# Optimization experiments

Measured on AMD Instinct MI355X. Metric: run time of the kernel, lower is better.

## Reference

```python
import jax, jax.numpy as jnp
import numpy as np

D_MODEL = 1024
H = 16
D_K = D_MODEL // H


def setup_inputs() -> dict:
    key = jax.random.key(0)
    ks = jax.random.split(key, 10)
    B, S = 2, 2048
    s = 1.0 / np.sqrt(D_MODEL)
    x = jax.random.normal(ks[0], (B, S, D_MODEL), dtype=jnp.float32)
    mask = jax.random.randint(ks[1], (B, 1, S, S), 0, 2, dtype=jnp.int32)
    w_q = jax.random.normal(ks[2], (D_MODEL, D_MODEL), dtype=jnp.float32) * s
    b_q = jnp.zeros((D_MODEL,), dtype=jnp.float32)
    w_k = jax.random.normal(ks[3], (D_MODEL, D_MODEL), dtype=jnp.float32) * s
    b_k = jnp.zeros((D_MODEL,), dtype=jnp.float32)
    w_v = jax.random.normal(ks[4], (D_MODEL, D_MODEL), dtype=jnp.float32) * s
    b_v = jnp.zeros((D_MODEL,), dtype=jnp.float32)
    w_o = jax.random.normal(ks[5], (D_MODEL, D_MODEL), dtype=jnp.float32) * s
    b_o = jnp.zeros((D_MODEL,), dtype=jnp.float32)
    return {"x": x, "mask": mask, "w_q": w_q, "b_q": b_q, "w_k": w_k,
            "b_k": b_k, "w_v": w_v, "b_v": b_v, "w_o": w_o, "b_o": b_o}


def reference(x, mask, w_q, b_q, w_k, b_k, w_v, b_v, w_o, b_o):
    B, S, _ = x.shape
    # projections; weights stored as (in, out) equivalents of torch Linear
    q = (x @ w_q + b_q).reshape(B, S, H, D_K).transpose(0, 2, 1, 3)  # bhsd
    k = (x @ w_k + b_k).reshape(B, S, H, D_K).transpose(0, 2, 1, 3)
    v = (x @ w_v + b_v).reshape(B, S, H, D_K).transpose(0, 2, 1, 3)
    scores = jnp.einsum('bhqd,bhkd->bhqk', q, k) / jnp.sqrt(jnp.float32(D_K))
    scores = jnp.where(mask == 0, jnp.float32(-1e9), scores)
    attn = jax.nn.softmax(scores, axis=-1)  # dropout omitted (eval mode)
    out = jnp.einsum('bhqk,bhkd->bhqd', attn, v)
    out = out.transpose(0, 2, 1, 3).reshape(B, S, D_MODEL)
    return out @ w_o + b_o
```

## Files before the change

### kernel.cpp

```cpp
#include <hip/hip_runtime.h>
#include <hip/hip_bf16.h>
#include <stdint.h>

#define D_MODEL 1024
#define NH 16
#define DK 64
#define SEQ 2048
#define BATCH 2
#define NTOK (BATCH * SEQ)

typedef __bf16 bf16;
typedef float f32x4 __attribute__((ext_vector_type(4)));
typedef __bf16 bf16x8 __attribute__((ext_vector_type(8)));
typedef __bf16 bf16x4 __attribute__((ext_vector_type(4)));

#define QSCALE 0.18033687932432668f

__device__ __forceinline__ void gload_lds16(const void* g, void* l) {
  __builtin_amdgcn_global_load_lds(
      (const __attribute__((address_space(1))) void*)g,
      (__attribute__((address_space(3))) void*)l, 16, 0, 0);
}

__global__ void prep_kernel(const float* __restrict__ x, bf16* __restrict__ xb,
                            const float* __restrict__ wq, const float* __restrict__ wk,
                            const float* __restrict__ wv, const float* __restrict__ wo,
                            bf16* __restrict__ wt,
                            const int* __restrict__ mask, unsigned long long* __restrict__ bits) {
  __shared__ float tile[32][33];
  const int bx = blockIdx.x;
  const int tid = threadIdx.x;
  if (bx < 4096) {
    int i = bx * 256 + tid;
    float4 v = reinterpret_cast<const float4*>(x)[i];
    bf16x4 o;
    o[0] = (bf16)v.x; o[1] = (bf16)v.y; o[2] = (bf16)v.z; o[3] = (bf16)v.w;
    reinterpret_cast<bf16x4*>(xb)[i] = o;
  } else if (bx < 8192) {
    int blk = bx - 4096;
    const int jt = blk & 127;
    const int kt = blk >> 7;
    const int tx = tid & 31, ty = tid >> 5;
    const int j0 = jt * 32;
    const int sel = j0 >> 10;
    const float* w = (sel == 0) ? wq : (sel == 1) ? wk : (sel == 2) ? wv : wo;
    const int jj0 = j0 & 1023;
#pragma unroll
    for (int i = 0; i < 4; ++i)
      tile[ty + i * 8][tx] = w[(size_t)(kt * 32 + ty + i * 8) * 1024 + jj0 + tx];
    __syncthreads();
#pragma unroll
    for (int i = 0; i < 4; ++i)
      wt[(size_t)(j0 + ty + i * 8) * 1024 + kt * 32 + tx] = (bf16)tile[tx][ty + i * 8];
  } else {
    int gt = (bx - 8192) * 256 + tid;
    int wid = gt >> 6;
    int l = gt & 63;
    int m = mask[(size_t)wid * 64 + l];
    unsigned long long b = __ballot(m != 0);
    if (l == 0) bits[wid] = b;
  }
}

__global__ __launch_bounds__(256) void gemm_qkv(
    const bf16* __restrict__ A, const bf16* __restrict__ Bt,
    const float* __restrict__ b0, const float* __restrict__ b1, const float* __restrict__ b2,
    bf16* __restrict__ out_q, bf16* __restrict__ out_k, bf16* __restrict__ out_vt) {
  __shared__ __align__(16) bf16 As[128 * 64];
  __shared__ __align__(16) bf16 Bs[128 * 64];
  const int tid = threadIdx.x;
  const int w = tid >> 6, l = tid & 63;
  const int wr = w >> 1, wc = w & 1;
  int lin = blockIdx.x + 24 * blockIdx.y;
  int xcd = lin & 7, idx = lin >> 3;
  const int n0 = (xcd * 3 + idx % 3) * 128;
  const int m0 = (idx / 3) * 128;
  f32x4 acc[4][4] = {};
  const int srow = w * 8 + (l >> 3);
  const int ssw = ((l & 7) ^ (l >> 3)) * 8;
  char* AsB = (char*)As;
  char* BsB = (char*)Bs;

  for (int k0 = 0; k0 < 1024; k0 += 64) {
#pragma unroll
    for (int i = 0; i < 4; ++i) {
      gload_lds16(A + (size_t)(m0 + i * 32 + srow) * 1024 + k0 + ssw, AsB + i * 4096 + w * 1024);
      gload_lds16(Bt + (size_t)(n0 + i * 32 + srow) * 1024 + k0 + ssw, BsB + i * 4096 + w * 1024);
    }
    __syncthreads();
#pragma unroll
    for (int kk = 0; kk < 2; ++kk) {
      const int cc = (((kk * 4 + (l >> 4)) ^ (l & 7)) << 3);
      bf16x8 af[4], bfr[4];
#pragma unroll
      for (int m = 0; m < 4; ++m)
        af[m] = *reinterpret_cast<const bf16x8*>(As + (wr * 64 + m * 16 + (l & 15)) * 64 + cc);
#pragma unroll
      for (int n = 0; n < 4; ++n)
        bfr[n] = *reinterpret_cast<const bf16x8*>(Bs + (wc * 64 + n * 16 + (l & 15)) * 64 + cc);
#pragma unroll
      for (int m = 0; m < 4; ++m)
#pragma unroll
        for (int n = 0; n < 4; ++n)
          acc[m][n] = __builtin_amdgcn_mfma_f32_16x16x32_bf16(af[m], bfr[n], acc[m][n], 0, 0, 0);
    }
    __syncthreads();
  }

#pragma unroll
  for (int m = 0; m < 4; ++m) {
    int ib = m0 + wr * 64 + m * 16 + 4 * (l >> 4);
#pragma unroll
    for (int n = 0; n < 4; ++n) {
      int j = n0 + wc * 64 + n * 16 + (l & 15);
      int sel = j >> 10, jj = j & 1023;
      const float* bp = (sel == 0) ? b0 : (sel == 1) ? b1 : b2;
      float bias = bp[jj];
      if (sel == 0) {
#pragma unroll
        for (int r = 0; r < 4; ++r)
          out_q[(size_t)(ib + r) * 1024 + jj] = (bf16)((acc[m][n][r] + bias) * QSCALE);
      } else if (sel == 1) {
#pragma unroll
        for (int r = 0; r < 4; ++r)
          out_k[(size_t)(ib + r) * 1024 + jj] = (bf16)(acc[m][n][r] + bias);
      } else {
        int hh = jj >> 6, dd = jj & 63;
        int bb = ib >> 11, ss = ib & 2047;
        bf16x4 v;
#pragma unroll
        for (int r = 0; r < 4; ++r) v[r] = (bf16)(acc[m][n][r] + bias);
        *reinterpret_cast<bf16x4*>(out_vt + ((size_t)(bb * NH + hh) * DK + dd) * SEQ + ss) = v;
      }
    }
  }
}

__global__ __launch_bounds__(256) void gemm_out(
    const bf16* __restrict__ A, const bf16* __restrict__ Bt,
    const float* __restrict__ bias, float* __restrict__ out) {
  __shared__ __align__(16) bf16 As[128 * 64];
  __shared__ __align__(16) bf16 Bs[64 * 64];
  const int tid = threadIdx.x;
  const int w = tid >> 6, l = tid & 63;
  const int wr = w >> 1, wc = w & 1;
  int lin = blockIdx.x + 16 * blockIdx.y;
  int xcd = lin & 7, idx = lin >> 3;
  const int n0 = (xcd * 2 + idx % 2) * 64;
  const int m0 = (idx / 2) * 128;
  f32x4 acc[4][2] = {};
  const int srow = w * 8 + (l >> 3);
  const int ssw = ((l & 7) ^ (l >> 3)) * 8;
  char* AsB = (char*)As;
  char* BsB = (char*)Bs;

  for (int k0 = 0; k0 < 1024; k0 += 64) {
#pragma unroll
    for (int i = 0; i < 4; ++i)
      gload_lds16(A + (size_t)(m0 + i * 32 + srow) * 1024 + k0 + ssw, AsB + i * 4096 + w * 1024);
#pragma unroll
    for (int i = 0; i < 2; ++i)
      gload_lds16(Bt + (size_t)(n0 + i * 32 + srow) * 1024 + k0 + ssw, BsB + i * 4096 + w * 1024);
    __syncthreads();
#pragma unroll
    for (int kk = 0; kk < 2; ++kk) {
      const int cc = (((kk * 4 + (l >> 4)) ^ (l & 7)) << 3);
      bf16x8 af[4], bfr[2];
#pragma unroll
      for (int m = 0; m < 4; ++m)
        af[m] = *reinterpret_cast<const bf16x8*>(As + (wr * 64 + m * 16 + (l & 15)) * 64 + cc);
#pragma unroll
      for (int n = 0; n < 2; ++n)
        bfr[n] = *reinterpret_cast<const bf16x8*>(Bs + (wc * 32 + n * 16 + (l & 15)) * 64 + cc);
#pragma unroll
      for (int m = 0; m < 4; ++m)
#pragma unroll
        for (int n = 0; n < 2; ++n)
          acc[m][n] = __builtin_amdgcn_mfma_f32_16x16x32_bf16(af[m], bfr[n], acc[m][n], 0, 0, 0);
    }
    __syncthreads();
  }

#pragma unroll
  for (int m = 0; m < 4; ++m) {
    int ib = m0 + wr * 64 + m * 16 + 4 * (l >> 4);
#pragma unroll
    for (int n = 0; n < 2; ++n) {
      int j = n0 + wc * 32 + n * 16 + (l & 15);
      float bv = bias[j];
#pragma unroll
      for (int r = 0; r < 4; ++r)
        out[(size_t)(ib + r) * 1024 + j] = acc[m][n][r] + bv;
    }
  }
}

__global__ __launch_bounds__(256, 4) void attn_kernel(
    const bf16* __restrict__ qb, const bf16* __restrict__ kb,
    const bf16* __restrict__ vt, const unsigned long long* __restrict__ mbits,
    bf16* __restrict__ ob) {
  __shared__ __align__(16) bf16 Kbuf[2][64 * 64];
  __shared__ __align__(16) bf16 Vbuf[2][64 * 64];
  __shared__ __align__(16) bf16 Ps[4][16 * 64];
  const int tid = threadIdx.x;
  const int w = tid >> 6, l = tid & 63;
  int lin = blockIdx.x + 32 * blockIdx.y + 512 * blockIdx.z;
  int nl = (lin & 7) * 128 + (lin >> 3);
  const int qt = nl & 31, h = (nl >> 5) & 15, b = nl >> 9;
  const int q0 = qt * 64;
  const int qrow = q0 + w * 16;
  const int tok0 = b * SEQ + qrow;
  const int a = l >> 4, c = l & 15;

  bf16x8 qf[2];
#pragma unroll
  for (int kk = 0; kk < 2; ++kk)
    qf[kk] = *reinterpret_cast<const bf16x8*>(
        qb + (size_t)(tok0 + c) * 1024 + h * 64 + kk * 32 + a * 8);

  float lsum = 0.f;
  f32x4 oacc[4] = {};

  const int swz = ((l & 7) ^ (l >> 3)) * 8;
  const bf16* ksrc = kb + (size_t)(b * SEQ) * 1024 + h * 64;
  const bf16* vsrc = vt + (size_t)(b * NH + h) * DK * SEQ;
  const unsigned long long* mrow = mbits + ((size_t)(b * SEQ + qrow + c) << 5);

  auto STAGE = [&](int buf, int kt) {
    char* KsB = (char*)Kbuf[buf];
    char* VsB = (char*)Vbuf[buf];
#pragma unroll
    for (int i = 0; i < 2; ++i) {
      int row = i * 32 + w * 8 + (l >> 3);
      gload_lds16(ksrc + (size_t)(kt * 64 + row) * 1024 + swz, KsB + i * 4096 + w * 1024);
      gload_lds16(vsrc + (size_t)row * SEQ + kt * 64 + swz, VsB + i * 4096 + w * 1024);
    }
  };

  STAGE(0, 0);
  for (int kt = 0; kt < 32; ++kt) {
    const int cur = kt & 1;
    unsigned long long mw = mrow[kt];
    __builtin_amdgcn_sched_barrier(0);
    if (kt < 31) {
      STAGE(cur ^ 1, kt + 1);
      __builtin_amdgcn_sched_barrier(0);
      asm volatile("s_waitcnt vmcnt(5)" ::: "memory");
    } else {
      __builtin_amdgcn_sched_barrier(0);
      asm volatile("s_waitcnt vmcnt(0)" ::: "memory");
    }
    __builtin_amdgcn_s_barrier();
    __builtin_amdgcn_sched_barrier(0);

    const bf16* Ks = Kbuf[cur];
    const bf16* Vs = Vbuf[cur];

    f32x4 sa[4] = {};
#pragma unroll
    for (int kk = 0; kk < 2; ++kk) {
      bf16x8 kf[4];
      int cc = kk * 4 + a;
#pragma unroll
      for (int n = 0; n < 4; ++n) {
        int rr = n * 16 + c;
        kf[n] = *reinterpret_cast<const bf16x8*>(Ks + rr * 64 + ((cc ^ (rr & 7)) << 3));
      }
#pragma unroll
      for (int n = 0; n < 4; ++n)
        sa[n] = __builtin_amdgcn_mfma_f32_16x16x32_bf16(kf[n], qf[kk], sa[n], 0, 0, 0);
    }

    unsigned long long base = mw >> (a * 4);
    float ps[4][4];
#pragma unroll
    for (int n = 0; n < 4; ++n)
#pragma unroll
      for (int r = 0; r < 4; ++r) {
        bool on = (base >> (16 * n + r)) & 1ull;
        float p = on ? __builtin_amdgcn_exp2f(sa[n][r]) : 0.f;
        ps[n][r] = p;
        lsum += p;
      }
#pragma unroll
    for (int n = 0; n < 4; ++n) {
      int chunk = (2 * n + (a >> 1)) ^ (c & 7);
      bf16x4 v4;
      v4[0] = (bf16)ps[n][0]; v4[1] = (bf16)ps[n][1];
      v4[2] = (bf16)ps[n][2]; v4[3] = (bf16)ps[n][3];
      *reinterpret_cast<bf16x4*>(Ps[w] + c * 64 + chunk * 8 + 4 * (a & 1)) = v4;
    }

#pragma unroll
    for (int kk = 0; kk < 2; ++kk) {
      bf16x8 pa = *reinterpret_cast<const bf16x8*>(Ps[w] + c * 64 + (((a + 4 * kk) ^ (c & 7)) << 3));
      bf16x8 vf[4];
#pragma unroll
      for (int dn = 0; dn < 4; ++dn) {
        int rr = dn * 16 + c;
        vf[dn] = *reinterpret_cast<const bf16x8*>(Vs + rr * 64 + (((kk * 4 + a) ^ (rr & 7)) << 3));
      }
#pragma unroll
      for (int dn = 0; dn < 4; ++dn)
        oacc[dn] = __builtin_amdgcn_mfma_f32_16x16x32_bf16(pa, vf[dn], oacc[dn], 0, 0, 0);
    }
    __builtin_amdgcn_sched_barrier(0);
    __builtin_amdgcn_s_barrier();
  }

  float s = lsum;
  s += __shfl_xor(s, 16);
  s += __shfl_xor(s, 32);
#pragma unroll
  for (int r = 0; r < 4; ++r) {
    float sr = __shfl(s, 4 * a + r);
    float inv = 1.f / fmaxf(sr, 1e-35f);
    int tok = tok0 + 4 * a + r;
#pragma unroll
    for (int dn = 0; dn < 4; ++dn)
      ob[(size_t)tok * 1024 + h * 64 + dn * 16 + c] = (bf16)(oacc[dn][r] * inv);
  }
}

extern "C" void kernel_launch(void* const* d_in, const int* in_sizes, int n_in,
                              void* d_out, int out_size, void* d_ws, size_t ws_size,
                              hipStream_t stream) {
  const float* x = (const float*)d_in[0];
  const int* mask = (const int*)d_in[1];
  const float* wq = (const float*)d_in[2];
  const float* bq = (const float*)d_in[3];
  const float* wk = (const float*)d_in[4];
  const float* bk = (const float*)d_in[5];
  const float* wv = (const float*)d_in[6];
  const float* bv = (const float*)d_in[7];
  const float* wo = (const float*)d_in[8];
  const float* bo = (const float*)d_in[9];
  float* out = (float*)d_out;

  char* ws = (char*)d_ws;
  bf16* xb = (bf16*)(ws + (size_t)0);
  bf16* wt = (bf16*)(ws + ((size_t)8 << 20));
  bf16* qb = (bf16*)(ws + ((size_t)16 << 20));
  bf16* kb = (bf16*)(ws + ((size_t)24 << 20));
  bf16* vtb = (bf16*)(ws + ((size_t)32 << 20));
  bf16* ob = (bf16*)(ws + ((size_t)40 << 20));
  unsigned long long* mbits = (unsigned long long*)(ws + ((size_t)48 << 20));

  prep_kernel<<<40960, 256, 0, stream>>>(x, xb, wq, wk, wv, wo, wt, mask, mbits);
  gemm_qkv<<<dim3(24, 32), 256, 0, stream>>>(xb, wt, bq, bk, bv, qb, kb, vtb);
  attn_kernel<<<dim3(32, NH, BATCH), 256, 0, stream>>>(qb, kb, vtb, mbits, ob);
  gemm_out<<<dim3(16, 32), 256, 0, stream>>>(ob, wt + (size_t)3072 * 1024, bo, out);
}
```

Measured before the change: 238.5 us.

## Double attention query tile to 128 rows and shrink GEMM K-tile to 32

```diff
diff --git a/kernel.cpp b/kernel.cpp
--- a/kernel.cpp
+++ b/kernel.cpp
@@ -66,8 +66,8 @@
     const bf16* __restrict__ A, const bf16* __restrict__ Bt,
     const float* __restrict__ b0, const float* __restrict__ b1, const float* __restrict__ b2,
     bf16* __restrict__ out_q, bf16* __restrict__ out_k, bf16* __restrict__ out_vt) {
-  __shared__ __align__(16) bf16 As[128 * 64];
-  __shared__ __align__(16) bf16 Bs[128 * 64];
+  __shared__ __align__(16) bf16 As[128 * 32];
+  __shared__ __align__(16) bf16 Bs[128 * 32];
   const int tid = threadIdx.x;
   const int w = tid >> 6, l = tid & 63;
   const int wr = w >> 1, wc = w & 1;
@@ -76,34 +76,32 @@
   const int n0 = (xcd * 3 + idx % 3) * 128;
   const int m0 = (idx / 3) * 128;
   f32x4 acc[4][4] = {};
-  const int srow = w * 8 + (l >> 3);
-  const int ssw = ((l & 7) ^ (l >> 3)) * 8;
+  const int lrow = l >> 2;
+  const int lc8 = (l & 3) * 8;
   char* AsB = (char*)As;
   char* BsB = (char*)Bs;
 
-  for (int k0 = 0; k0 < 1024; k0 += 64) {
-#pragma unroll
-    for (int i = 0; i < 4; ++i) {
-      gload_lds16(A + (size_t)(m0 + i * 32 + srow) * 1024 + k0 + ssw, AsB + i * 4096 + w * 1024);
-      gload_lds16(Bt + (size_t)(n0 + i * 32 + srow) * 1024 + k0 + ssw, BsB + i * 4096 + w * 1024);
-    }
-    __syncthreads();
-#pragma unroll
-    for (int kk = 0; kk < 2; ++kk) {
-      const int cc = (((kk * 4 + (l >> 4)) ^ (l & 7)) << 3);
-      bf16x8 af[4], bfr[4];
-#pragma unroll
-      for (int m = 0; m < 4; ++m)
-        af[m] = *reinterpret_cast<const bf16x8*>(As + (wr * 64 + m * 16 + (l & 15)) * 64 + cc);
+  for (int k0 = 0; k0 < 1024; k0 += 32) {
+#pragma unroll
+    for (int is = 0; is < 2; ++is) {
+      int arow = m0 + is * 64 + w * 16 + lrow;
+      gload_lds16(A + (size_t)arow * 1024 + k0 + lc8, AsB + is * 4096 + w * 1024);
+      int brow = n0 + is * 64 + w * 16 + lrow;
+      gload_lds16(Bt + (size_t)brow * 1024 + k0 + lc8, BsB + is * 4096 + w * 1024);
+    }
+    __syncthreads();
+    bf16x8 af[4], bfr[4];
+#pragma unroll
+    for (int m = 0; m < 4; ++m)
+      af[m] = *reinterpret_cast<const bf16x8*>(As + (wr * 64 + m * 16 + (l & 15)) * 32 + (l >> 4) * 8);
+#pragma unroll
+    for (int n = 0; n < 4; ++n)
+      bfr[n] = *reinterpret_cast<const bf16x8*>(Bs + (wc * 64 + n * 16 + (l & 15)) * 32 + (l >> 4) * 8);
+#pragma unroll
+    for (int m = 0; m < 4; ++m)
 #pragma unroll
       for (int n = 0; n < 4; ++n)
-        bfr[n] = *reinterpret_cast<const bf16x8*>(Bs + (wc * 64 + n * 16 + (l & 15)) * 64 + cc);
-#pragma unroll
-      for (int m = 0; m < 4; ++m)
-#pragma unroll
-        for (int n = 0; n < 4; ++n)
-          acc[m][n] = __builtin_amdgcn_mfma_f32_16x16x32_bf16(af[m], bfr[n], acc[m][n], 0, 0, 0);
-    }
+        acc[m][n] = __builtin_amdgcn_mfma_f32_16x16x32_bf16(af[m], bfr[n], acc[m][n], 0, 0, 0);
     __syncthreads();
   }
 
@@ -139,8 +137,8 @@
 __global__ __launch_bounds__(256) void gemm_out(
     const bf16* __restrict__ A, const bf16* __restrict__ Bt,
     const float* __restrict__ bias, float* __restrict__ out) {
-  __shared__ __align__(16) bf16 As[128 * 64];
-  __shared__ __align__(16) bf16 Bs[64 * 64];
+  __shared__ __align__(16) bf16 As[128 * 32];
+  __shared__ __align__(16) bf16 Bs[64 * 32];
   const int tid = threadIdx.x;
   const int w = tid >> 6, l = tid & 63;
   const int wr = w >> 1, wc = w & 1;
@@ -149,35 +147,31 @@
   const int n0 = (xcd * 2 + idx % 2) * 64;
   const int m0 = (idx / 2) * 128;
   f32x4 acc[4][2] = {};
-  const int srow = w * 8 + (l >> 3);
-  const int ssw = ((l & 7) ^ (l >> 3)) * 8;
+  const int lrow = l >> 2;
+  const int lc8 = (l & 3) * 8;
   char* AsB = (char*)As;
   char* BsB = (char*)Bs;
 
-  for (int k0 = 0; k0 < 1024; k0 += 64) {
-#pragma unroll
-    for (int i = 0; i < 4; ++i)
-      gload_lds16(A + (size_t)(m0 + i * 32 + srow) * 1024 + k0 + ssw, AsB + i * 4096 + w * 1024);
-#pragma unroll
-    for (int i = 0; i < 2; ++i)
-      gload_lds16(Bt + (size_t)(n0 + i * 32 + srow) * 1024 + k0 + ssw, BsB + i * 4096 + w * 1024);
-    __syncthreads();
-#pragma unroll
-    for (int kk = 0; kk < 2; ++kk) {
-      const int cc = (((kk * 4 + (l >> 4)) ^ (l & 7)) << 3);
-      bf16x8 af[4], bfr[2];
-#pragma unroll
-      for (int m = 0; m < 4; ++m)
-        af[m] = *reinterpret_cast<const bf16x8*>(As + (wr * 64 + m * 16 + (l & 15)) * 64 + cc);
+  for (int k0 = 0; k0 < 1024; k0 += 32) {
+#pragma unroll
+    for (int is = 0; is < 2; ++is) {
+      int arow = m0 + is * 64 + w * 16 + lrow;
+      gload_lds16(A + (size_t)arow * 1024 + k0 + lc8, AsB + is * 4096 + w * 1024);
+    }
+    gload_lds16(Bt + (size_t)(n0 + w * 16 + lrow) * 1024 + k0 + lc8, BsB + w * 1024);
+    __syncthreads();
+    bf16x8 af[4], bfr[2];
+#pragma unroll
+    for (int m = 0; m < 4; ++m)
+      af[m] = *reinterpret_cast<const bf16x8*>(As + (wr * 64 + m * 16 + (l & 15)) * 32 + (l >> 4) * 8);
+#pragma unroll
+    for (int n = 0; n < 2; ++n)
+      bfr[n] = *reinterpret_cast<const bf16x8*>(Bs + (wc * 32 + n * 16 + (l & 15)) * 32 + (l >> 4) * 8);
+#pragma unroll
+    for (int m = 0; m < 4; ++m)
 #pragma unroll
       for (int n = 0; n < 2; ++n)
-        bfr[n] = *reinterpret_cast<const bf16x8*>(Bs + (wc * 32 + n * 16 + (l & 15)) * 64 + cc);
-#pragma unroll
-      for (int m = 0; m < 4; ++m)
-#pragma unroll
-        for (int n = 0; n < 2; ++n)
-          acc[m][n] = __builtin_amdgcn_mfma_f32_16x16x32_bf16(af[m], bfr[n], acc[m][n], 0, 0, 0);
-    }
+        acc[m][n] = __builtin_amdgcn_mfma_f32_16x16x32_bf16(af[m], bfr[n], acc[m][n], 0, 0, 0);
     __syncthreads();
   }
 
@@ -195,20 +189,19 @@
   }
 }
 
-__global__ __launch_bounds__(256, 4) void attn_kernel(
+__global__ __launch_bounds__(512, 4) void attn_kernel(
     const bf16* __restrict__ qb, const bf16* __restrict__ kb,
     const bf16* __restrict__ vt, const unsigned long long* __restrict__ mbits,
     bf16* __restrict__ ob) {
   __shared__ __align__(16) bf16 Kbuf[2][64 * 64];
   __shared__ __align__(16) bf16 Vbuf[2][64 * 64];
-  __shared__ __align__(16) bf16 Ps[4][16 * 64];
+  __shared__ __align__(16) bf16 Ps[8][16 * 64];
   const int tid = threadIdx.x;
   const int w = tid >> 6, l = tid & 63;
-  int lin = blockIdx.x + 32 * blockIdx.y + 512 * blockIdx.z;
-  int nl = (lin & 7) * 128 + (lin >> 3);
-  const int qt = nl & 31, h = (nl >> 5) & 15, b = nl >> 9;
-  const int q0 = qt * 64;
-  const int qrow = q0 + w * 16;
+  int lin = blockIdx.x + 16 * blockIdx.y + 256 * blockIdx.z;
+  int nl = (lin & 7) * 64 + (lin >> 3);
+  const int qt = nl & 15, h = (nl >> 4) & 15, b = nl >> 8;
+  const int qrow = qt * 128 + w * 16;
   const int tok0 = b * SEQ + qrow;
   const int a = l >> 4, c = l & 15;
 
@@ -227,13 +220,20 @@
   const unsigned long long* mrow = mbits + ((size_t)(b * SEQ + qrow + c) << 5);
 
   auto STAGE = [&](int buf, int kt) {
-    char* KsB = (char*)Kbuf[buf];
-    char* VsB = (char*)Vbuf[buf];
-#pragma unroll
-    for (int i = 0; i < 2; ++i) {
-      int row = i * 32 + w * 8 + (l >> 3);
-      gload_lds16(ksrc + (size_t)(kt * 64 + row) * 1024 + swz, KsB + i * 4096 + w * 1024);
-      gload_lds16(vsrc + (size_t)row * SEQ + kt * 64 + swz, VsB + i * 4096 + w * 1024);
+    if (w < 4) {
+      char* KsB = (char*)Kbuf[buf];
+#pragma unroll
+      for (int i = 0; i < 2; ++i) {
+        int row = w * 16 + i * 8 + (l >> 3);
+        gload_lds16(ksrc + (size_t)(kt * 64 + row) * 1024 + swz, KsB + w * 2048 + i * 1024);
+      }
+    } else {
+      char* VsB = (char*)Vbuf[buf];
+#pragma unroll
+      for (int i = 0; i < 2; ++i) {
+        int row = (w - 4) * 16 + i * 8 + (l >> 3);
+        gload_lds16(vsrc + (size_t)row * SEQ + kt * 64 + swz, VsB + (w - 4) * 2048 + i * 1024);
+      }
     }
   };
 
@@ -245,10 +245,10 @@
     if (kt < 31) {
       STAGE(cur ^ 1, kt + 1);
       __builtin_amdgcn_sched_barrier(0);
-      asm volatile("s_waitcnt vmcnt(5)" ::: "memory");
+      asm volatile("s_waitcnt vmcnt(3)" ::: "memory");
     } else {
       __builtin_amdgcn_sched_barrier(0);
-      asm volatile("s_waitcnt vmcnt(0)" ::: "memory");
+      asm volatile("s_waitcnt vmcnt(1)" ::: "memory");
     }
     __builtin_amdgcn_s_barrier();
     __builtin_amdgcn_sched_barrier(0);
@@ -348,6 +348,6 @@
 
   prep_kernel<<<40960, 256, 0, stream>>>(x, xb, wq, wk, wv, wo, wt, mask, mbits);
   gemm_qkv<<<dim3(24, 32), 256, 0, stream>>>(xb, wt, bq, bk, bv, qb, kb, vtb);
-  attn_kernel<<<dim3(32, NH, BATCH), 256, 0, stream>>>(qb, kb, vtb, mbits, ob);
+  attn_kernel<<<dim3(16, NH, BATCH), 512, 0, stream>>>(qb, kb, vtb, mbits, ob);
   gemm_out<<<dim3(16, 32), 256, 0, stream>>>(ob, wt + (size_t)3072 * 1024, bo, out);
 }
```

Measured after the change: 233.2 us. -2.2%, faster.
